# Kernel tuning notes

Measured on AMD Instinct MI355X. Metric: run time of the kernel, lower is better.

The kernel has to match this reference:

```python
import jax, jax.numpy as jnp
import numpy as np

N = 100000      # nodes
E = 1600000     # edges (avg degree 16)
IN_C = 128
HID = 64
OUT_C = 2


def compute_norm(edge_index, n):
    """1/rowcount of M = I + A^T (distinct nonzeros per row, coalesce semantics)."""
    idt = edge_index.dtype
    ar = jnp.arange(n, dtype=idt)
    rows = jnp.concatenate([ar, edge_index[1]])  # M built from transposed edges
    cols = jnp.concatenate([ar, edge_index[0]])
    order = jnp.lexsort((cols, rows))
    rs, cs = rows[order], cols[order]
    uniq = jnp.concatenate([jnp.array([True]),
                            (rs[1:] != rs[:-1]) | (cs[1:] != cs[:-1])])
    rowcount = jnp.zeros((n,), jnp.float32).at[rs].add(uniq.astype(jnp.float32))
    return 1.0 / jnp.maximum(rowcount, 1.0)


def pan_conv(x, edge_index, w_lin, b_lin, w_pan, norm):
    # PyG PANConv, filter_size=1: out = diag(norm) @ (w0*I + w0*w1*A^T) @ (x W + b)
    h = x @ w_lin + b_lin                                   # [N, HID]
    src, dst = edge_index[0], edge_index[1]
    agg = jnp.zeros_like(h).at[dst].add(h[src])             # (A^T h)[i] = sum_{src->i} h[src]
    out = w_pan[0] * h + (w_pan[0] * w_pan[1]) * agg
    return norm[:, None] * out


def setup_inputs() -> dict:
    key = jax.random.key(0)
    ks = jax.random.split(key, 8)
    x = jax.random.normal(ks[0], (N, IN_C), jnp.float32)
    edge_index = jax.random.randint(ks[1], (2, E), 0, N, dtype=jnp.int32)
    w1_lin = jax.random.normal(ks[2], (IN_C, HID), jnp.float32) * 0.05
    b1_lin = jnp.zeros((HID,), jnp.float32)
    w1_pan = jax.random.uniform(ks[3], (2,), jnp.float32, 0.5, 1.5)
    w2_lin = jax.random.normal(ks[4], (HID, HID), jnp.float32) * 0.05
    b2_lin = jnp.zeros((HID,), jnp.float32)
    w2_pan = jax.random.uniform(ks[5], (2,), jnp.float32, 0.5, 1.5)
    wc = jax.random.normal(ks[6], (2 * HID, OUT_C), jnp.float32) * 0.05
    bc = jnp.zeros((OUT_C,), jnp.float32)
    return {"x": x, "edge_index": edge_index,
            "w1_lin": w1_lin, "b1_lin": b1_lin, "w1_pan": w1_pan,
            "w2_lin": w2_lin, "b2_lin": b2_lin, "w2_pan": w2_pan,
            "wc": wc, "bc": bc}


def reference(x, edge_index, w1_lin, b1_lin, w1_pan, w2_lin, b2_lin, w2_pan, wc, bc):
    n = x.shape[0]
    norm = compute_norm(edge_index, n)          # graph-structure only; shared by both layers
    h = pan_conv(x, edge_index, w1_lin, b1_lin, w1_pan, norm)
    h = jax.nn.relu(h)
    h = pan_conv(h, edge_index, w2_lin, b2_lin, w2_pan, norm)
    row, col = edge_index[0], edge_index[1]
    emb = jnp.concatenate([h[row], h[col]], axis=-1)  # [E, 2*HID]
    return emb @ wc + bc                               # [E, OUT_C]
```

## Files before the change

kernel.cpp:

```cpp
#include <hip/hip_runtime.h>
#include <hip/hip_bf16.h>

#define NNODES 100000
#define NEDGES 1600000
#define INC 128
#define HIDC 64
#define BSHIFT 8
#define NB ((NNODES + 255) / 256)
#define TILE 8192
#define HSLOTS 8192
#define CAP 8192
#define CAPE 8192
#define NBLK_FILL ((NEDGES + TILE - 1) / TILE)
#define NBLK_LIN ((NNODES + 63) / 64)

typedef short bf16x8 __attribute__((ext_vector_type(8)));
typedef float f32x4 __attribute__((ext_vector_type(4)));

__device__ __forceinline__ float bf2f(unsigned short h) {
    return __uint_as_float((unsigned)h << 16);
}
__device__ __forceinline__ unsigned short f2bf(float f) {
    __hip_bfloat16 h = __float2bfloat16(f);
    return *(unsigned short*)&h;
}

__global__ __launch_bounds__(256) void prep_w_kernel(
        const float* __restrict__ w1, unsigned short* __restrict__ wTh,
        unsigned short* __restrict__ wTl,
        const float* __restrict__ w2_lin, const float* __restrict__ b2,
        const float* __restrict__ wc, float* __restrict__ w44,
        float* __restrict__ bias4, unsigned short* __restrict__ out) {
    int t = threadIdx.x;
    int e = blockIdx.x * 256 + t;
    int c = e >> 7, k = e & 127;
    float v = w1[k * 64 + c];
    unsigned short hi = f2bf(v);
    wTh[e] = hi;
    wTl[e] = f2bf(v - bf2f(hi));
    if (blockIdx.x == 0) {
        if (t < 16)
            *(ushort4*)(out + (size_t)NNODES * 64 + t * 4) = make_ushort4(0, 0, 0, 0);
        int kk = t >> 2, j = t & 3;
        float a = 0.0f;
#pragma unroll 8
        for (int i = 0; i < 64; i++) {
            float w4 = (j < 2) ? wc[i * 2 + j] : wc[(64 + i) * 2 + (j - 2)];
            a += w2_lin[kk * 64 + i] * w4;
        }
        w44[kk * 4 + j] = a;
        if (kk == 0) {
            float bb4 = 0.0f;
            for (int i = 0; i < 64; i++) {
                float w4 = (j < 2) ? wc[i * 2 + j] : wc[(64 + i) * 2 + (j - 2)];
                bb4 += b2[i] * w4;
            }
            bias4[j] = bb4;
        }
    }
}

__global__ __launch_bounds__(256) void fat_kernel(
        const float* __restrict__ x,
        const unsigned short* __restrict__ wTh, const unsigned short* __restrict__ wTl,
        const float* __restrict__ b, unsigned short* __restrict__ out,
        const int* __restrict__ src, const int* __restrict__ dst,
        int* __restrict__ bucket_fill, unsigned int* __restrict__ staging) {
    __shared__ alignas(16) unsigned short s_a[2][64 * 128];
    __shared__ alignas(16) unsigned short s_b[2][64 * 128];
    int t = threadIdx.x;
    if (blockIdx.x < NBLK_FILL) {
        int* cnt = (int*)&s_a[0][0];
        int* basepos = cnt + NB;
        unsigned int* svl = (unsigned int*)&s_b[0][0];
        for (int i = t; i < NB; i += 256) cnt[i] = 0;
        __syncthreads();
        int tile0 = blockIdx.x * TILE;
        int meta[32];
#pragma unroll
        for (int i = 0; i < 32; i++) {
            int e = tile0 + i * 256 + t;
            meta[i] = -1;
            if (e < NEDGES) {
                int s = src[e], d = dst[e];
                int bkt = d >> BSHIFT;
                int r = atomicAdd(&cnt[bkt], 1);
                meta[i] = (bkt << 13) | r;
                svl[i * 256 + t] = ((unsigned)(d & 255) << 17) | (unsigned)s;
            }
        }
        __syncthreads();
        for (int i = t; i < NB; i += 256) {
            int c = cnt[i];
            int g = (c > 0) ? atomicAdd(&bucket_fill[i], c) : 0;
            basepos[i] = (i << 13) + g;
        }
        __syncthreads();
#pragma unroll
        for (int i = 0; i < 32; i++) {
            if (meta[i] >= 0) {
                int bkt = meta[i] >> 13, r = meta[i] & 8191;
                staging[basepos[bkt] + r] = svl[i * 256 + t];
            }
        }
    } else {
        int node0 = (blockIdx.x - NBLK_FILL) * 64;
        float4 vx[8];
#pragma unroll
        for (int it = 0; it < 8; it++) {
            int idx = it * 256 + t;
            int row = idx >> 5, c4 = idx & 31;
            int node = node0 + row;
            if (node < NNODES)
                vx[it] = *(const float4*)(x + (size_t)node * INC + c4 * 4);
            else
                vx[it] = make_float4(0.f, 0.f, 0.f, 0.f);
        }
        uint4 vwh[4], vwl[4];
#pragma unroll
        for (int j = 0; j < 4; j++) {
            vwh[j] = *(const uint4*)(wTh + (size_t)(j * 256 + t) * 8);
            vwl[j] = *(const uint4*)(wTl + (size_t)(j * 256 + t) * 8);
        }
#pragma unroll
        for (int it = 0; it < 8; it++) {
            int idx = it * 256 + t;
            int row = idx >> 5, c4 = idx & 31;
            ushort4 hi, lo;
            hi.x = f2bf(vx[it].x); lo.x = f2bf(vx[it].x - bf2f(hi.x));
            hi.y = f2bf(vx[it].y); lo.y = f2bf(vx[it].y - bf2f(hi.y));
            hi.z = f2bf(vx[it].z); lo.z = f2bf(vx[it].z - bf2f(hi.z));
            hi.w = f2bf(vx[it].w); lo.w = f2bf(vx[it].w - bf2f(hi.w));
            int ke = (c4 * 4) ^ ((row & 7) << 3);
            *(ushort4*)&s_a[0][row * 128 + ke] = hi;
            *(ushort4*)&s_a[1][row * 128 + ke] = lo;
        }
#pragma unroll
        for (int j = 0; j < 4; j++) {
            int idx = j * 256 + t;
            int col = idx >> 4, k0 = (idx & 15) * 8;
            int ke = k0 ^ ((col & 7) << 3);
            *(uint4*)&s_b[0][col * 128 + ke] = vwh[j];
            *(uint4*)&s_b[1][col * 128 + ke] = vwl[j];
        }
        __syncthreads();
        int l = t & 63, wv = t >> 6;
        int mr = l & 15, g = l >> 4;
        int arow = wv * 16 + mr;
        f32x4 acc[4] = {{0.f, 0.f, 0.f, 0.f}, {0.f, 0.f, 0.f, 0.f},
                        {0.f, 0.f, 0.f, 0.f}, {0.f, 0.f, 0.f, 0.f}};
#pragma unroll
        for (int ks = 0; ks < 4; ks++) {
            int k0 = ks * 32 + g * 8;
            int ko = k0 ^ ((mr & 7) << 3);
            bf16x8 ah = *(const bf16x8*)&s_a[0][arow * 128 + ko];
            bf16x8 al = *(const bf16x8*)&s_a[1][arow * 128 + ko];
#pragma unroll
            for (int cb = 0; cb < 4; cb++) {
                int bo = (cb * 16 + mr) * 128 + ko;
                bf16x8 bh = *(const bf16x8*)&s_b[0][bo];
                bf16x8 bl = *(const bf16x8*)&s_b[1][bo];
                acc[cb] = __builtin_amdgcn_mfma_f32_16x16x32_bf16(ah, bh, acc[cb], 0, 0, 0);
                acc[cb] = __builtin_amdgcn_mfma_f32_16x16x32_bf16(ah, bl, acc[cb], 0, 0, 0);
                acc[cb] = __builtin_amdgcn_mfma_f32_16x16x32_bf16(al, bh, acc[cb], 0, 0, 0);
            }
        }
#pragma unroll
        for (int cb = 0; cb < 4; cb++) {
            int col = cb * 16 + mr;
            float bb = b[col];
#pragma unroll
            for (int r = 0; r < 4; r++) {
                int node = node0 + wv * 16 + g * 4 + r;
                if (node < NNODES)
                    out[(size_t)node * 64 + col] = f2bf(acc[cb][r] + bb);
            }
        }
    }
}

__global__ __launch_bounds__(256) void fill2_kernel(
        const int* __restrict__ bucket_fill, const unsigned int* __restrict__ staging,
        int* __restrict__ csr_src, int* __restrict__ row_start,
        int* __restrict__ row_pdeg, float* __restrict__ norm, int n_nodes) {
    __shared__ int cnt[256];
    __shared__ int dcount[256];
    __shared__ int off[256];
    __shared__ int pscan[256];
    __shared__ unsigned short rank16[CAP];
    __shared__ unsigned int ht[HSLOTS];
    int t = threadIdx.x;
    int b = blockIdx.x;
    int node0 = b << BSHIFT;
    int nn = min(256, n_nodes - node0);
    cnt[t] = 0; dcount[t] = 0;
    {
        uint4* h4 = (uint4*)ht;
        uint4 ff = make_uint4(0xFFFFFFFFu, 0xFFFFFFFFu, 0xFFFFFFFFu, 0xFFFFFFFFu);
        for (int i = t; i < HSLOTS / 4; i += 256) h4[i] = ff;
    }
    __syncthreads();
    int start = b << 13;
    int total = bucket_fill[b];
    for (int li = t; li < total; li += 256) {
        unsigned int w = staging[start + li];
        int s = (int)(w & 0x1FFFFu);
        int dl = (int)(w >> 17);
        int r = atomicAdd(&cnt[dl], 1);
        rank16[li] = (unsigned short)r;
        if (s != node0 + dl) {
            unsigned int slot = ((w * 2654435761u) >> 13) & (HSLOTS - 1);
            while (true) {
                unsigned int prev = atomicCAS(&ht[slot], 0xFFFFFFFFu, w);
                if (prev == 0xFFFFFFFFu) { atomicAdd(&dcount[dl], 1); break; }
                if (prev == w) break;
                slot = (slot + 1) & (HSLOTS - 1);
            }
        }
    }
    __syncthreads();
    int cv = cnt[t];
    int pv = (cv + 7) & ~7;
    pscan[t] = pv;
    __syncthreads();
    for (int o = 1; o < 256; o <<= 1) {
        int xx = (t >= o) ? pscan[t - o] : 0;
        __syncthreads();
        pscan[t] += xx;
        __syncthreads();
    }
    off[t] = b * CAPE + pscan[t] - pv;
    __syncthreads();
    if (t < nn) {
        row_start[node0 + t] = off[t];
        row_pdeg[node0 + t] = pv;
        norm[node0 + t] = 1.0f / (1.0f + (float)dcount[t]);
    }
    for (int k = cv; k < pv; k++) csr_src[off[t] + k] = n_nodes << 7;
    for (int li = t; li < total; li += 256) {
        unsigned int w = staging[start + li];
        int s = (int)(w & 0x1FFFFu);
        int dl = (int)(w >> 17);
        csr_src[off[dl] + (int)rank16[li]] = s << 7;
    }
}

__global__ void agg_h_kernel(const unsigned int* __restrict__ lin32,
                             const int* __restrict__ row_start,
                             const int* __restrict__ row_pdeg,
                             const int* __restrict__ csr_src,
                             const float* __restrict__ norm,
                             const float* __restrict__ wpan, const float* __restrict__ w44,
                             const float* __restrict__ bias4, float* __restrict__ u,
                             int n_nodes) {
    int t = threadIdx.x;
    int lane = t & 63;
    int sl = lane & 31;
    int h5 = lane >> 5;
    int pair = blockIdx.x * 4 + (t >> 6);
    int node = pair * 2 + h5;
    if (blockIdx.x == 0 && t < 4) u[n_nodes * 4 + t] = 0.0f;
    if (pair * 2 >= n_nodes) return;
    bool valid = (node < n_nodes);
    int nc = valid ? node : 0;
    int e0 = row_start[nc];
    int pd = valid ? row_pdeg[nc] : 0;
    int pmax = max(pd, __shfl_xor(pd, 32));
    int sentB = n_nodes << 7;
    unsigned sl4 = (unsigned)sl * 4;
    const char* base8 = (const char*)lin32;
    float aLo0 = 0.f, aHi0 = 0.f, aLo1 = 0.f, aHi1 = 0.f;
    for (int base = 0; base < pmax; base += 32) {
        int li = base + sl;
        int so = (li < pd) ? csr_src[e0 + li] : sentB;
        int m = min(32, pmax - base);
#pragma unroll
        for (int i = 0; i < 32; i += 2) {
            if (i < m) {
                int sA0 = __builtin_amdgcn_readlane(so, i);
                int sB0 = __builtin_amdgcn_readlane(so, 32 + i);
                int sA1 = __builtin_amdgcn_readlane(so, i + 1);
                int sB1 = __builtin_amdgcn_readlane(so, 33 + i);
                int so0 = h5 ? sB0 : sA0;
                int so1 = h5 ? sB1 : sA1;
                unsigned int wd0 = *(const unsigned int*)(base8 + (unsigned)(so0 + sl4));
                unsigned int wd1 = *(const unsigned int*)(base8 + (unsigned)(so1 + sl4));
                aLo0 += __uint_as_float(wd0 << 16);
                aHi0 += __uint_as_float(wd0 & 0xFFFF0000u);
                aLo1 += __uint_as_float(wd1 << 16);
                aHi1 += __uint_as_float(wd1 & 0xFFFF0000u);
            }
        }
    }
    float accLo = aLo0 + aLo1;
    float accHi = aHi0 + aHi1;
    unsigned int wself = *(const unsigned int*)(base8 + (unsigned)((nc << 7) + sl4));
    float nr = norm[nc];
    float w0 = wpan[0];
    float w01 = wpan[0] * wpan[1];
    float vLo = fmaxf(nr * (w0 * __uint_as_float(wself << 16) + w01 * accLo), 0.0f);
    float vHi = fmaxf(nr * (w0 * __uint_as_float(wself & 0xFFFF0000u) + w01 * accHi), 0.0f);
    int c0 = 2 * sl;
    float4 wv0 = *(const float4*)(w44 + c0 * 4);
    float4 wv1 = *(const float4*)(w44 + (c0 + 1) * 4);
    float p0 = vLo * wv0.x + vHi * wv1.x;
    float p1 = vLo * wv0.y + vHi * wv1.y;
    float p2 = vLo * wv0.z + vHi * wv1.z;
    float p3 = vLo * wv0.w + vHi * wv1.w;
    for (int off = 16; off; off >>= 1) {
        p0 += __shfl_xor(p0, off);
        p1 += __shfl_xor(p1, off);
        p2 += __shfl_xor(p2, off);
        p3 += __shfl_xor(p3, off);
    }
    if (sl == 0 && valid) {
        float4 bb = *(const float4*)bias4;
        *(float4*)(u + node * 4) =
            make_float4(p0 + bb.x, p1 + bb.y, p2 + bb.z, p3 + bb.w);
    }
}

__global__ void agg_pq4_kernel(const float* __restrict__ u, const int* __restrict__ row_start,
                               const int* __restrict__ row_pdeg,
                               const int* __restrict__ csr_src,
                               const float* __restrict__ norm,
                               const float* __restrict__ wpan, float* __restrict__ pq,
                               int n_nodes) {
    int t = threadIdx.x;
    int node = blockIdx.x * 64 + (t >> 2);
    int j = t & 3;
    if (node >= n_nodes) return;
    int e0 = row_start[node];
    int pd = row_pdeg[node];
    float acc = 0.0f;
    for (int e = 0; e < pd; e += 8) {
#pragma unroll
        for (int k = 0; k < 8; k++) {
            int so = csr_src[e0 + e + k];
            acc += u[(so >> 5) + j];
        }
    }
    float w0 = wpan[0];
    float w01 = wpan[0] * wpan[1];
    pq[node * 4 + j] = norm[node] * (w0 * u[node * 4 + j] + w01 * acc);
}

__global__ void edge_out_kernel(const int* __restrict__ src, const int* __restrict__ dst,
                                const float* __restrict__ pq, const float* __restrict__ bc,
                                float* __restrict__ out, int n_edges) {
    int e = blockIdx.x * blockDim.x + threadIdx.x;
    if (e >= n_edges) return;
    int r = src[e], c = dst[e];
    float2 p = *(const float2*)(pq + r * 4);
    float2 q = *(const float2*)(pq + c * 4 + 2);
    float2 o = make_float2(p.x + q.x + bc[0], p.y + q.y + bc[1]);
    *(float2*)(out + e * 2) = o;
}

extern "C" void kernel_launch(void* const* d_in, const int* in_sizes, int n_in,
                              void* d_out, int out_size, void* d_ws, size_t ws_size,
                              hipStream_t stream) {
    const float* x      = (const float*)d_in[0];
    const int*   eidx   = (const int*)d_in[1];
    const float* w1_lin = (const float*)d_in[2];
    const float* b1_lin = (const float*)d_in[3];
    const float* w1_pan = (const float*)d_in[4];
    const float* w2_lin = (const float*)d_in[5];
    const float* b2_lin = (const float*)d_in[6];
    const float* w2_pan = (const float*)d_in[7];
    const float* wc     = (const float*)d_in[8];
    const float* bc     = (const float*)d_in[9];
    float* out = (float*)d_out;

    const int* src = eidx;
    const int* dst = eidx + NEDGES;

    char* ws = (char*)d_ws;
    size_t off = 0;
    auto carve = [&](size_t bytes) {
        char* p = ws + off;
        off = (off + bytes + 255) & ~(size_t)255;
        return p;
    };
    int*   bucket_fill = (int*)carve((size_t)NB * 4);
    int*   row_start = (int*)carve((size_t)NNODES * 4);
    int*   row_pdeg  = (int*)carve((size_t)NNODES * 4);
    unsigned int* staging = (unsigned int*)carve((size_t)NB * CAP * 4);
    int*   csr_src  = (int*)carve(((size_t)NB * CAPE + 256) * 4);
    float* nrm      = (float*)carve((size_t)NNODES * 4);
    unsigned short* bufA = (unsigned short*)carve((size_t)(NNODES + 1) * HIDC * 2);
    float* u        = (float*)carve((size_t)(NNODES + 1) * 4 * 4);
    float* pq       = (float*)carve((size_t)NNODES * 4 * 4);
    float* w44      = (float*)carve((size_t)64 * 4 * 4);
    float* bias4    = (float*)carve((size_t)4 * 4);
    unsigned short* wTh = (unsigned short*)carve((size_t)HIDC * INC * 2);
    unsigned short* wTl = (unsigned short*)carve((size_t)HIDC * INC * 2);
    (void)ws_size; (void)in_sizes; (void)n_in; (void)out_size;

    hipMemsetAsync(bucket_fill, 0, (size_t)NB * 4, stream);

    prep_w_kernel<<<32, 256, 0, stream>>>(w1_lin, wTh, wTl, w2_lin, b2_lin, wc,
                                          w44, bias4, bufA);

    fat_kernel<<<NBLK_FILL + NBLK_LIN, 256, 0, stream>>>(
        x, wTh, wTl, b1_lin, bufA, src, dst, bucket_fill, staging);

    fill2_kernel<<<NB, 256, 0, stream>>>(bucket_fill, staging, csr_src, row_start, row_pdeg,
                                         nrm, NNODES);

    agg_h_kernel<<<(NNODES + 7) / 8, 256, 0, stream>>>(
        (const unsigned int*)bufA, row_start, row_pdeg, csr_src, nrm, w1_pan, w44, bias4,
        u, NNODES);

    agg_pq4_kernel<<<(NNODES + 63) / 64, 256, 0, stream>>>(
        u, row_start, row_pdeg, csr_src, nrm, w2_pan, pq, NNODES);

    edge_out_kernel<<<NEDGES / 256, 256, 0, stream>>>(src, dst, pq, bc, out, NEDGES);
}
```

Baseline: 244.0 us.

## Halve CSR bucket size and process four nodes per wave in aggregation

Bucket granularity drops from 256 to 128 nodes, so fill tiles, hash tables and staging capacity are halved. That doubles the number of bucketing blocks and reduces shared memory per block, which could raise occupancy in fill2. The first aggregation kernel now handles two nodes per half-wave instead of one, giving more independent gathers in flight per wave and half as many blocks. The range checks for nodes past the end are removed, which relies on N being divisible by 16, and buckets with unusually high degree risk overflowing the smaller capacity.

Result: faster. 233.0 us (-4.5%).

```diff
diff --git a/kernel.cpp b/kernel.cpp
--- a/kernel.cpp
+++ b/kernel.cpp
@@ -5,12 +5,12 @@
 #define NEDGES 1600000
 #define INC 128
 #define HIDC 64
-#define BSHIFT 8
-#define NB ((NNODES + 255) / 256)
-#define TILE 8192
-#define HSLOTS 8192
-#define CAP 8192
-#define CAPE 8192
+#define BSHIFT 7
+#define NB ((NNODES + 127) / 128)
+#define TILE 4096
+#define HSLOTS 4096
+#define CAP 4096
+#define CAPE 4096
 #define NBLK_FILL ((NEDGES + TILE - 1) / TILE)
 #define NBLK_LIN ((NNODES + 63) / 64)
 
@@ -76,30 +76,30 @@
         for (int i = t; i < NB; i += 256) cnt[i] = 0;
         __syncthreads();
         int tile0 = blockIdx.x * TILE;
-        int meta[32];
-#pragma unroll
-        for (int i = 0; i < 32; i++) {
+        int meta[16];
+#pragma unroll
+        for (int i = 0; i < 16; i++) {
             int e = tile0 + i * 256 + t;
             meta[i] = -1;
             if (e < NEDGES) {
                 int s = src[e], d = dst[e];
                 int bkt = d >> BSHIFT;
                 int r = atomicAdd(&cnt[bkt], 1);
-                meta[i] = (bkt << 13) | r;
-                svl[i * 256 + t] = ((unsigned)(d & 255) << 17) | (unsigned)s;
+                meta[i] = (bkt << 12) | r;
+                svl[i * 256 + t] = ((unsigned)(d & 127) << 17) | (unsigned)s;
             }
         }
         __syncthreads();
         for (int i = t; i < NB; i += 256) {
             int c = cnt[i];
             int g = (c > 0) ? atomicAdd(&bucket_fill[i], c) : 0;
-            basepos[i] = (i << 13) + g;
-        }
-        __syncthreads();
-#pragma unroll
-        for (int i = 0; i < 32; i++) {
+            basepos[i] = (i << 12) + g;
+        }
+        __syncthreads();
+#pragma unroll
+        for (int i = 0; i < 16; i++) {
             if (meta[i] >= 0) {
-                int bkt = meta[i] >> 13, r = meta[i] & 8191;
+                int bkt = meta[i] >> 12, r = meta[i] & 4095;
                 staging[basepos[bkt] + r] = svl[i * 256 + t];
             }
         }
@@ -183,24 +183,24 @@
         const int* __restrict__ bucket_fill, const unsigned int* __restrict__ staging,
         int* __restrict__ csr_src, int* __restrict__ row_start,
         int* __restrict__ row_pdeg, float* __restrict__ norm, int n_nodes) {
-    __shared__ int cnt[256];
-    __shared__ int dcount[256];
-    __shared__ int off[256];
-    __shared__ int pscan[256];
+    __shared__ int cnt[128];
+    __shared__ int dcount[128];
+    __shared__ int off[128];
+    __shared__ int pscan[128];
     __shared__ unsigned short rank16[CAP];
     __shared__ unsigned int ht[HSLOTS];
     int t = threadIdx.x;
     int b = blockIdx.x;
     int node0 = b << BSHIFT;
-    int nn = min(256, n_nodes - node0);
-    cnt[t] = 0; dcount[t] = 0;
+    int nn = min(128, n_nodes - node0);
+    if (t < 128) { cnt[t] = 0; dcount[t] = 0; }
     {
         uint4* h4 = (uint4*)ht;
         uint4 ff = make_uint4(0xFFFFFFFFu, 0xFFFFFFFFu, 0xFFFFFFFFu, 0xFFFFFFFFu);
         for (int i = t; i < HSLOTS / 4; i += 256) h4[i] = ff;
     }
     __syncthreads();
-    int start = b << 13;
+    int start = b << 12;
     int total = bucket_fill[b];
     for (int li = t; li < total; li += 256) {
         unsigned int w = staging[start + li];
@@ -219,24 +219,28 @@
         }
     }
     __syncthreads();
-    int cv = cnt[t];
-    int pv = (cv + 7) & ~7;
-    pscan[t] = pv;
+    int cv = 0, pv = 0;
+    if (t < 128) {
+        cv = cnt[t];
+        pv = (cv + 7) & ~7;
+        pscan[t] = pv;
+    }
     __syncthreads();
-    for (int o = 1; o < 256; o <<= 1) {
-        int xx = (t >= o) ? pscan[t - o] : 0;
-        __syncthreads();
-        pscan[t] += xx;
-        __syncthreads();
-    }
-    off[t] = b * CAPE + pscan[t] - pv;
+    for (int o = 1; o < 128; o <<= 1) {
+        int xx = (t >= o && t < 128) ? pscan[t - o] : 0;
+        __syncthreads();
+        if (t < 128) pscan[t] += xx;
+        __syncthreads();
+    }
+    if (t < 128) off[t] = b * CAPE + pscan[t] - pv;
     __syncthreads();
     if (t < nn) {
         row_start[node0 + t] = off[t];
         row_pdeg[node0 + t] = pv;
         norm[node0 + t] = 1.0f / (1.0f + (float)dcount[t]);
     }
-    for (int k = cv; k < pv; k++) csr_src[off[t] + k] = n_nodes << 7;
+    if (t < 128)
+        for (int k = cv; k < pv; k++) csr_src[off[t] + k] = n_nodes << 7;
     for (int li = t; li < total; li += 256) {
         unsigned int w = staging[start + li];
         int s = (int)(w & 0x1FFFFu);
@@ -257,66 +261,95 @@
     int lane = t & 63;
     int sl = lane & 31;
     int h5 = lane >> 5;
-    int pair = blockIdx.x * 4 + (t >> 6);
-    int node = pair * 2 + h5;
+    int quad = blockIdx.x * 4 + (t >> 6);
     if (blockIdx.x == 0 && t < 4) u[n_nodes * 4 + t] = 0.0f;
-    if (pair * 2 >= n_nodes) return;
-    bool valid = (node < n_nodes);
-    int nc = valid ? node : 0;
-    int e0 = row_start[nc];
-    int pd = valid ? row_pdeg[nc] : 0;
-    int pmax = max(pd, __shfl_xor(pd, 32));
+    int nX = quad * 4 + h5 * 2;
+    int nY = nX + 1;
+    int e0X = row_start[nX], pdX = row_pdeg[nX];
+    int e0Y = row_start[nY], pdY = row_pdeg[nY];
+    int pm = max(pdX, pdY);
+    int pmax = max(pm, __shfl_xor(pm, 32));
     int sentB = n_nodes << 7;
     unsigned sl4 = (unsigned)sl * 4;
     const char* base8 = (const char*)lin32;
-    float aLo0 = 0.f, aHi0 = 0.f, aLo1 = 0.f, aHi1 = 0.f;
+    float xL0 = 0.f, xH0 = 0.f, xL1 = 0.f, xH1 = 0.f;
+    float yL0 = 0.f, yH0 = 0.f, yL1 = 0.f, yH1 = 0.f;
     for (int base = 0; base < pmax; base += 32) {
         int li = base + sl;
-        int so = (li < pd) ? csr_src[e0 + li] : sentB;
+        int soX = (li < pdX) ? csr_src[e0X + li] : sentB;
+        int soY = (li < pdY) ? csr_src[e0Y + li] : sentB;
         int m = min(32, pmax - base);
 #pragma unroll
         for (int i = 0; i < 32; i += 2) {
             if (i < m) {
-                int sA0 = __builtin_amdgcn_readlane(so, i);
-                int sB0 = __builtin_amdgcn_readlane(so, 32 + i);
-                int sA1 = __builtin_amdgcn_readlane(so, i + 1);
-                int sB1 = __builtin_amdgcn_readlane(so, 33 + i);
-                int so0 = h5 ? sB0 : sA0;
-                int so1 = h5 ? sB1 : sA1;
-                unsigned int wd0 = *(const unsigned int*)(base8 + (unsigned)(so0 + sl4));
-                unsigned int wd1 = *(const unsigned int*)(base8 + (unsigned)(so1 + sl4));
-                aLo0 += __uint_as_float(wd0 << 16);
-                aHi0 += __uint_as_float(wd0 & 0xFFFF0000u);
-                aLo1 += __uint_as_float(wd1 << 16);
-                aHi1 += __uint_as_float(wd1 & 0xFFFF0000u);
-            }
-        }
-    }
-    float accLo = aLo0 + aLo1;
-    float accHi = aHi0 + aHi1;
-    unsigned int wself = *(const unsigned int*)(base8 + (unsigned)((nc << 7) + sl4));
-    float nr = norm[nc];
+                int xA0 = __builtin_amdgcn_readlane(soX, i);
+                int xB0 = __builtin_amdgcn_readlane(soX, 32 + i);
+                int xA1 = __builtin_amdgcn_readlane(soX, i + 1);
+                int xB1 = __builtin_amdgcn_readlane(soX, 33 + i);
+                int yA0 = __builtin_amdgcn_readlane(soY, i);
+                int yB0 = __builtin_amdgcn_readlane(soY, 32 + i);
+                int yA1 = __builtin_amdgcn_readlane(soY, i + 1);
+                int yB1 = __builtin_amdgcn_readlane(soY, 33 + i);
+                int ox0 = h5 ? xB0 : xA0;
+                int ox1 = h5 ? xB1 : xA1;
+                int oy0 = h5 ? yB0 : yA0;
+                int oy1 = h5 ? yB1 : yA1;
+                unsigned int wx0 = *(const unsigned int*)(base8 + (unsigned)(ox0 + sl4));
+                unsigned int wx1 = *(const unsigned int*)(base8 + (unsigned)(ox1 + sl4));
+                unsigned int wy0 = *(const unsigned int*)(base8 + (unsigned)(oy0 + sl4));
+                unsigned int wy1 = *(const unsigned int*)(base8 + (unsigned)(oy1 + sl4));
+                xL0 += __uint_as_float(wx0 << 16);
+                xH0 += __uint_as_float(wx0 & 0xFFFF0000u);
+                xL1 += __uint_as_float(wx1 << 16);
+                xH1 += __uint_as_float(wx1 & 0xFFFF0000u);
+                yL0 += __uint_as_float(wy0 << 16);
+                yH0 += __uint_as_float(wy0 & 0xFFFF0000u);
+                yL1 += __uint_as_float(wy1 << 16);
+                yH1 += __uint_as_float(wy1 & 0xFFFF0000u);
+            }
+        }
+    }
+    float aLX = xL0 + xL1, aHX = xH0 + xH1;
+    float aLY = yL0 + yL1, aHY = yH0 + yH1;
+    unsigned int wsX = *(const unsigned int*)(base8 + (unsigned)((nX << 7) + sl4));
+    unsigned int wsY = *(const unsigned int*)(base8 + (unsigned)((nY << 7) + sl4));
+    float nrX = norm[nX], nrY = norm[nY];
     float w0 = wpan[0];
     float w01 = wpan[0] * wpan[1];
-    float vLo = fmaxf(nr * (w0 * __uint_as_float(wself << 16) + w01 * accLo), 0.0f);
-    float vHi = fmaxf(nr * (w0 * __uint_as_float(wself & 0xFFFF0000u) + w01 * accHi), 0.0f);
+    float vLX = fmaxf(nrX * (w0 * __uint_as_float(wsX << 16) + w01 * aLX), 0.0f);
+    float vHX = fmaxf(nrX * (w0 * __uint_as_float(wsX & 0xFFFF0000u) + w01 * aHX), 0.0f);
+    float vLY = fmaxf(nrY * (w0 * __uint_as_float(wsY << 16) + w01 * aLY), 0.0f);
+    float vHY = fmaxf(nrY * (w0 * __uint_as_float(wsY & 0xFFFF0000u) + w01 * aHY), 0.0f);
     int c0 = 2 * sl;
     float4 wv0 = *(const float4*)(w44 + c0 * 4);
     float4 wv1 = *(const float4*)(w44 + (c0 + 1) * 4);
-    float p0 = vLo * wv0.x + vHi * wv1.x;
-    float p1 = vLo * wv0.y + vHi * wv1.y;
-    float p2 = vLo * wv0.z + vHi * wv1.z;
-    float p3 = vLo * wv0.w + vHi * wv1.w;
+    float pX0 = vLX * wv0.x + vHX * wv1.x;
+    float pX1 = vLX * wv0.y + vHX * wv1.y;
+    float pX2 = vLX * wv0.z + vHX * wv1.z;
+    float pX3 = vLX * wv0.w + vHX * wv1.w;
+    float pY0 = vLY * wv0.x + vHY * wv1.x;
+    float pY1 = vLY * wv0.y + vHY * wv1.y;
+    float pY2 = vLY * wv0.z + vHY * wv1.z;
+    float pY3 = vLY * wv0.w + vHY * wv1.w;
     for (int off = 16; off; off >>= 1) {
-        p0 += __shfl_xor(p0, off);
-        p1 += __shfl_xor(p1, off);
-        p2 += __shfl_xor(p2, off);
-        p3 += __shfl_xor(p3, off);
-    }
-    if (sl == 0 && valid) {
+        pX0 += __shfl_xor(pX0, off);
+        pX1 += __shfl_xor(pX1, off);
+        pX2 += __shfl_xor(pX2, off);
+        pX3 += __shfl_xor(pX3, off);
+        pY0 += __shfl_xor(pY0, off);
+        pY1 += __shfl_xor(pY1, off);
+        pY2 += __shfl_xor(pY2, off);
+        pY3 += __shfl_xor(pY3, off);
+    }
+    if (sl == 0) {
         float4 bb = *(const float4*)bias4;
-        *(float4*)(u + node * 4) =
-            make_float4(p0 + bb.x, p1 + bb.y, p2 + bb.z, p3 + bb.w);
+        *(float4*)(u + nX * 4) =
+            make_float4(pX0 + bb.x, pX1 + bb.y, pX2 + bb.z, pX3 + bb.w);
+    }
+    if (sl == 1) {
+        float4 bb = *(const float4*)bias4;
+        *(float4*)(u + nY * 4) =
+            make_float4(pY0 + bb.x, pY1 + bb.y, pY2 + bb.z, pY3 + bb.w);
     }
 }
 
@@ -408,7 +441,7 @@
     fill2_kernel<<<NB, 256, 0, stream>>>(bucket_fill, staging, csr_src, row_start, row_pdeg,
                                          nrm, NNODES);
 
-    agg_h_kernel<<<(NNODES + 7) / 8, 256, 0, stream>>>(
+    agg_h_kernel<<<(NNODES / 16), 256, 0, stream>>>(
         (const unsigned int*)bufA, row_start, row_pdeg, csr_src, nrm, w1_pan, w44, bias4,
         u, NNODES);
 
```
